# Performance work log

Measured on AMD Instinct MI355X. Metric: run time of the kernel, lower is better.

## Reference

```python
import jax, jax.numpy as jnp
import numpy as np

N, D, C = 8192, 256, 100
MARGIN = 1.0


def setup_inputs() -> dict:
    key = jax.random.key(0)
    k1, k2 = jax.random.split(key)
    features = jax.random.normal(k1, (N, D), dtype=jnp.float32)
    labels = jax.random.randint(k2, (N,), 0, C, dtype=jnp.int64)
    return {"features": features, "labels": labels}


def _pairwise_dist(f):
    # f: [N, D] L2-normalized rows. Euclidean distance matrix [N, N].
    sq = jnp.sum(f * f, axis=1)  # [N]
    d2 = sq[:, None] + sq[None, :] - 2.0 * (f @ f.T)
    d2 = jnp.maximum(d2, 0.0)
    # safe sqrt: zero distance (incl. diagonal) -> 0 with finite grad
    pos = d2 > 0.0
    return jnp.where(pos, jnp.sqrt(jnp.where(pos, d2, 1.0)), 0.0)


def reference(features, labels):
    # F.normalize(p=2, dim=1)
    norm = jnp.linalg.norm(features, axis=1, keepdims=True)
    f = features / jnp.maximum(norm, 1e-12)

    dist = _pairwise_dist(f)  # [N, N]

    onehot = jax.nn.one_hot(labels, C, dtype=f.dtype)  # [N, C]
    counts = jnp.sum(onehot, axis=0)  # [C]
    # S[a, b] = sum_{i in a, j in b} dist[i, j]
    S = onehot.T @ dist @ onehot  # [C, C]

    # intra: per-class mean over off-diagonal pairs (diag of dist is 0),
    # only classes with count > 1, then mean over those classes
    intra_valid = counts > 1.0
    intra_denom = jnp.where(intra_valid, counts * (counts - 1.0), 1.0)
    intra_per_class = jnp.diag(S) / intra_denom
    n_intra = jnp.sum(intra_valid.astype(f.dtype))
    intra = jnp.where(
        n_intra > 0,
        jnp.sum(jnp.where(intra_valid, intra_per_class, 0.0)) / jnp.maximum(n_intra, 1.0),
        0.0,
    )

    # inter: per class-pair (a < b, both present) mean distance, then mean over pairs
    pair_cnt = counts[:, None] * counts[None, :]
    inter_mat = S / jnp.where(pair_cnt > 0.0, pair_cnt, 1.0)
    present = counts > 0.0
    upper = jnp.triu(jnp.ones((C, C), dtype=bool), k=1)
    pair_mask = upper & present[:, None] & present[None, :]
    n_pairs = jnp.sum(pair_mask.astype(f.dtype))
    inter = jnp.where(
        n_pairs > 0,
        jnp.sum(jnp.where(pair_mask, inter_mat, 0.0)) / jnp.maximum(n_pairs, 1.0),
        1.0,
    )

    loss = jax.nn.relu(intra - inter + MARGIN)
    return loss  # scalar; .mean() of a scalar is itself
```

## Files before the change

### kernel.cpp

```cpp
#include <hip/hip_runtime.h>
#include <math.h>

#define N_ROWS 8192
#define D_DIM  256
#define C_CLS  100
#define BM 128
#define BK 128
#define NSTRIP (N_ROWS / BM)
#define NBLK (NSTRIP * (NSTRIP + 1) / 2)
#define UPK (C_CLS * (C_CLS + 1) / 2)
#define MAXSEG 4

typedef __attribute__((ext_vector_type(4))) float floatx4;

__device__ __forceinline__ void gl2lds16(const void* g, void* l) {
    __builtin_amdgcn_global_load_lds(
        (const __attribute__((address_space(1))) void*)g,
        (__attribute__((address_space(3))) void*)l, 16, 0, 0);
}

__global__ void sort_k(const int* __restrict__ labels, int* __restrict__ dest,
                       int* __restrict__ slab, int* __restrict__ offs,
                       float* __restrict__ Ug) {
    __shared__ int h[C_CLS];
    __shared__ int incl[128];
    __shared__ int oS[C_CLS + 1];
    __shared__ int cur[C_CLS];
    const int t = threadIdx.x;
    if (t < C_CLS) h[t] = 0;
    __syncthreads();
    int myl[8];
#pragma unroll
    for (int u = 0; u < 8; ++u) myl[u] = labels[t + u * 1024];
#pragma unroll
    for (int u = 0; u < 8; ++u) atomicAdd(&h[myl[u]], 1);
    __syncthreads();
    if (t < 128) {
        const int lane = t & 63;
        int v = (t < C_CLS) ? h[t] : 0;
#pragma unroll
        for (int o = 1; o < 64; o <<= 1) {
            const int n = __shfl_up(v, o, 64);
            if (lane >= o) v += n;
        }
        incl[t] = v;
    }
    __syncthreads();
    if (t <= C_CLS)
        oS[t] = (t == 0) ? 0 : incl[t - 1] + ((t - 1) >= 64 ? incl[63] : 0);
    __syncthreads();
    if (t < C_CLS) cur[t] = oS[t];
    __syncthreads();
#pragma unroll
    for (int u = 0; u < 8; ++u) {
        const int i = t + u * 1024;
        const int pos = atomicAdd(&cur[myl[u]], 1);
        dest[i] = pos;
        slab[pos] = myl[u];
    }
    if (t < C_CLS + 1) offs[t] = oS[t];
    for (int e = t; e < UPK; e += 1024) Ug[e] = 0.f;
}

__global__ void normalize_k(const float* __restrict__ in, const int* __restrict__ dest,
                            unsigned int* __restrict__ fnb8) {
    const int row  = blockIdx.x * 4 + (threadIdx.x >> 6);
    const int lane = threadIdx.x & 63;
    float4 v = ((const float4*)in)[row * 64 + lane];
    float s = v.x * v.x + v.y * v.y + v.z * v.z + v.w * v.w;
#pragma unroll
    for (int o = 32; o > 0; o >>= 1) s += __shfl_xor(s, o, 64);
    const float inv = 1.f / fmaxf(sqrtf(s), 1e-12f);
    const int d = dest[row];
    int pk = __builtin_amdgcn_cvt_pk_fp8_f32(v.x * inv, v.y * inv, 0, 0);
    pk     = __builtin_amdgcn_cvt_pk_fp8_f32(v.z * inv, v.w * inv, pk, 1);
    fnb8[d * 64 + lane] = (unsigned int)pk;
}

__global__ __launch_bounds__(256, 4)
void main_k(const unsigned char* __restrict__ fnb8, const int* __restrict__ slab,
            const int* __restrict__ offs_g, float* __restrict__ Ug) {
    __shared__ __align__(16) unsigned char As[BM * BK];
    __shared__ __align__(16) unsigned char Bs[BM * BK];
    __shared__ float red[4][MAXSEG * MAXSEG][17];
    __shared__ int soffs[C_CLS + 1];
    __shared__ int meta[4][4];

    const int t = threadIdx.x;

    int b = (blockIdx.x & 7) * (NBLK / 8) + (blockIdx.x >> 3);
    int ti = 0, len = NSTRIP;
    while (b >= len) { b -= len; ++ti; --len; }
    const int tj = ti + b;
    const int i0 = ti * BM, j0 = tj * BM;

    if (t < C_CLS + 1) soffs[t] = offs_g[t];

    const int lane = t & 63;
    const int w    = t >> 6;
    const int m0 = (w & 1) * 64, n0 = (w >> 1) * 64;
    const int lr = lane & 15, lq = lane >> 4;
    const int swz = (lr >> 1) & 7;

    int abase[4], bbase[4];
#pragma unroll
    for (int mb = 0; mb < 4; ++mb) abase[mb] = (m0 + mb * 16 + lr) * BK;
#pragma unroll
    for (int nb = 0; nb < 4; ++nb) bbase[nb] = (n0 + nb * 16 + lr) * BK;

    int srow[4], skc[4];
#pragma unroll
    for (int u = 0; u < 4; ++u) {
        const int s = t + 256 * u;
        srow[u] = s >> 3;
        skc[u]  = (s & 7) ^ ((srow[u] >> 1) & 7);
    }

    floatx4 acc[4][4];
#pragma unroll
    for (int mb = 0; mb < 4; ++mb)
#pragma unroll
        for (int nb = 0; nb < 4; ++nb) acc[mb][nb] = 0.f;

#pragma unroll
    for (int k0 = 0; k0 < D_DIM; k0 += BK) {
        __syncthreads();
#pragma unroll
        for (int u = 0; u < 4; ++u)
            gl2lds16(&fnb8[(size_t)(i0 + srow[u]) * D_DIM + k0 + skc[u] * 16],
                     &As[(t + 256 * u) * 16]);
#pragma unroll
        for (int u = 0; u < 4; ++u)
            gl2lds16(&fnb8[(size_t)(j0 + srow[u]) * D_DIM + k0 + skc[u] * 16],
                     &Bs[(t + 256 * u) * 16]);
        __syncthreads();

#pragma unroll
        for (int si = 0; si < 4; ++si) {
            const int coff = ((((si * 2) + (lq >> 1)) ^ swz) << 4) + ((lq & 1) << 3);
            long a[4], bb[4];
#pragma unroll
            for (int mb = 0; mb < 4; ++mb) a[mb]  = *(const long*)&As[abase[mb] + coff];
#pragma unroll
            for (int nb = 0; nb < 4; ++nb) bb[nb] = *(const long*)&Bs[bbase[nb] + coff];
#pragma unroll
            for (int mb = 0; mb < 4; ++mb)
#pragma unroll
                for (int nb = 0; nb < 4; ++nb)
                    acc[mb][nb] = __builtin_amdgcn_mfma_f32_16x16x32_fp8_fp8(
                        a[mb], bb[nb], acc[mb][nb], 0, 0, 0);
        }
    }

    const bool diag = (ti == tj);
#pragma unroll
    for (int mb = 0; mb < 4; ++mb)
#pragma unroll
        for (int nb = 0; nb < 4; ++nb)
#pragma unroll
            for (int r = 0; r < 4; ++r) {
                const float g = acc[mb][nb][r];
                float dv = __builtin_amdgcn_sqrtf(fmaxf(2.f - 2.f * g, 0.f));
                const int rt = m0 + mb * 16 + lq * 4 + r;
                const int ct = n0 + nb * 16 + lr;
                if (diag && rt == ct) dv = 0.f;
                acc[mb][nb][r] = dv;
            }

    const int cA0 = __builtin_amdgcn_readfirstlane(slab[i0 + m0]);
    const int cA1 = __builtin_amdgcn_readfirstlane(slab[i0 + m0 + 63]);
    const int cB0 = __builtin_amdgcn_readfirstlane(slab[j0 + n0]);
    const int cB1 = __builtin_amdgcn_readfirstlane(slab[j0 + n0 + 63]);
    const int segsA = cA1 - cA0 + 1, segsB = cB1 - cB0 + 1;
    if (lane == 0) {
        meta[w][0] = cA0; meta[w][1] = cB0; meta[w][2] = segsA; meta[w][3] = segsB;
    }
    const float wscale = diag ? 1.f : 2.f;

    float rem[4][4];
#pragma unroll
    for (int mb = 0; mb < 4; ++mb)
#pragma unroll
        for (int r = 0; r < 4; ++r)
            rem[mb][r] = acc[mb][0][r] + acc[mb][1][r] + acc[mb][2][r] + acc[mb][3][r];

    for (int sb = 0; sb < segsB; ++sb) {
        const int cb = cB0 + sb;
        float colsum[4][4];
        if (sb == segsB - 1) {
#pragma unroll
            for (int mb = 0; mb < 4; ++mb)
#pragma unroll
                for (int r = 0; r < 4; ++r) colsum[mb][r] = rem[mb][r];
        } else {
            const int rb0 = max(soffs[cb]     - j0, n0);
            const int rb1 = min(soffs[cb + 1] - j0, n0 + 64);
#pragma unroll
            for (int mb = 0; mb < 4; ++mb)
#pragma unroll
                for (int r = 0; r < 4; ++r) colsum[mb][r] = 0.f;
#pragma unroll
            for (int nb = 0; nb < 4; ++nb) {
                const int ct = n0 + nb * 16 + lr;
                const float mk = ((ct >= rb0) & (ct < rb1)) ? 1.f : 0.f;
#pragma unroll
                for (int mb = 0; mb < 4; ++mb)
#pragma unroll
                    for (int r = 0; r < 4; ++r)
                        colsum[mb][r] = fmaf(mk, acc[mb][nb][r], colsum[mb][r]);
            }
#pragma unroll
            for (int mb = 0; mb < 4; ++mb)
#pragma unroll
                for (int r = 0; r < 4; ++r) rem[mb][r] -= colsum[mb][r];
        }
        for (int sa = 0; sa < segsA; ++sa) {
            const int ca = cA0 + sa;
            const int ra0 = max(soffs[ca]     - i0, m0);
            const int ra1 = min(soffs[ca + 1] - i0, m0 + 64);
            float v = 0.f;
#pragma unroll
            for (int mb = 0; mb < 4; ++mb) {
                const int rtb = m0 + mb * 16 + lq * 4;
#pragma unroll
                for (int r = 0; r < 4; ++r) {
                    const int rt = rtb + r;
                    const bool ir = (rt >= ra0) & (rt < ra1);
                    v += ir ? colsum[mb][r] : 0.f;
                }
            }
            if (sa < MAXSEG && sb < MAXSEG) {
                v += __shfl_xor(v, 1, 64);
                v += __shfl_xor(v, 2, 64);
                if ((lane & 3) == 0) red[w][sb * MAXSEG + sa][lane >> 2] = v;
            } else {
#pragma unroll
                for (int o = 32; o > 0; o >>= 1) v += __shfl_xor(v, o, 64);
                if (lane == 0 && v != 0.f) {
                    const int mn = min(ca, cb), mx = max(ca, cb);
                    atomicAdd(&Ug[mx + ((mn * (2 * C_CLS - 1 - mn)) >> 1)], wscale * v);
                }
            }
        }
    }

    __syncthreads();
    {
        const int combo = t >> 2, q = t & 3;
        const int wv = combo >> 4, sl = combo & 15;
        float s = red[wv][sl][q * 4 + 0] + red[wv][sl][q * 4 + 1]
                + red[wv][sl][q * 4 + 2] + red[wv][sl][q * 4 + 3];
        s += __shfl_xor(s, 1, 64);
        s += __shfl_xor(s, 2, 64);
        const int sa = sl & (MAXSEG - 1), sb = sl >> 2;
        if (q == 0 && sa < meta[wv][2] && sb < meta[wv][3] && s != 0.f) {
            const float wscale2 = meta[wv][0] == meta[wv][1] && m0 == n0 ? 0.f : 0.f;
            (void)wscale2;
            const int ca = meta[wv][0] + sa, cb = meta[wv][1] + sb;
            const int mn = min(ca, cb), mx = max(ca, cb);
            atomicAdd(&Ug[mx + ((mn * (2 * C_CLS - 1 - mn)) >> 1)], wscale * s);
        }
    }
}

__global__ void finalize_k(const float* __restrict__ U, const int* __restrict__ offs,
                           float* __restrict__ out) {
    __shared__ int   cnt[C_CLS];
    __shared__ float rf[256];
    __shared__ int   ri[256];
    const int t = threadIdx.x;
    if (t < C_CLS) cnt[t] = offs[t + 1] - offs[t];
    __syncthreads();

    float s_intra = 0.f; int n_intra = 0;
    if (t < C_CLS) {
        int c = cnt[t];
        if (c > 1) {
            int idx = t + ((t * (2 * C_CLS - 1 - t)) >> 1);
            s_intra = U[idx] / ((float)c * (float)(c - 1));
            n_intra = 1;
        }
    }
    float s_inter = 0.f; int n_pairs = 0;
    for (int p = t; p < C_CLS * C_CLS; p += 256) {
        int a = p / C_CLS, b2 = p - a * C_CLS;
        if (b2 > a && cnt[a] > 0 && cnt[b2] > 0) {
            int idx = b2 + ((a * (2 * C_CLS - 1 - a)) >> 1);
            s_inter += 0.5f * U[idx] / ((float)cnt[a] * (float)cnt[b2]);
            ++n_pairs;
        }
    }

    rf[t] = s_intra; ri[t] = n_intra; __syncthreads();
    for (int s = 128; s > 0; s >>= 1) {
        if (t < s) { rf[t] += rf[t + s]; ri[t] += ri[t + s]; }
        __syncthreads();
    }
    float intra_sum = rf[0]; int intra_n = ri[0];
    __syncthreads();
    rf[t] = s_inter; ri[t] = n_pairs; __syncthreads();
    for (int s = 128; s > 0; s >>= 1) {
        if (t < s) { rf[t] += rf[t + s]; ri[t] += ri[t + s]; }
        __syncthreads();
    }
    if (t == 0) {
        float inter_sum = rf[0]; int pairs_n = ri[0];
        float intra = (intra_n > 0) ? intra_sum / (float)intra_n : 0.f;
        float inter = (pairs_n > 0) ? inter_sum / (float)pairs_n : 1.f;
        out[0] = fmaxf(intra - inter + 1.0f, 0.f);
    }
}

extern "C" void kernel_launch(void* const* d_in, const int* in_sizes, int n_in,
                              void* d_out, int out_size, void* d_ws, size_t ws_size,
                              hipStream_t stream) {
    const float* feats  = (const float*)d_in[0];
    const int*   labels = (const int*)d_in[1];
    float* out = (float*)d_out;

    char* p = (char*)d_ws;
    unsigned char* fnb8 = (unsigned char*)p;  p += (size_t)N_ROWS * D_DIM;
    int*   slab = (int*)p;  p += (size_t)N_ROWS * sizeof(int);
    int*   dest = (int*)p;  p += (size_t)N_ROWS * sizeof(int);
    int*   offs = (int*)p;  p += 128 * sizeof(int);
    float* Ug   = (float*)p;

    sort_k     <<<1, 1024, 0, stream>>>(labels, dest, slab, offs, Ug);
    normalize_k<<<N_ROWS / 4, 256, 0, stream>>>(feats, dest, (unsigned int*)fnb8);
    main_k     <<<NBLK, 256, 0, stream>>>(fnb8, slab, offs, Ug);
    finalize_k <<<1, 256, 0, stream>>>(Ug, offs, out);
}
```

Baseline: 109.7 us.

## Double-buffer LDS K tiles with BK=64 to overlap loads and MFMA

Halves the K tile to 64 bytes and double-buffers the A/B LDS tiles. The next K chunk is issued via global_load_lds while MFMAs run on the current one, over four K steps instead of two. This is meant to hide global-load latency behind compute. The swizzle and load mapping are adjusted for the narrower tile. The final reduction now computes its weight inline from the diagonal-tile test instead of using wscale, which may change semantics if wscale differed.

```diff
diff --git a/kernel.cpp b/kernel.cpp
--- a/kernel.cpp
+++ b/kernel.cpp
@@ -5,7 +5,7 @@
 #define D_DIM  256
 #define C_CLS  100
 #define BM 128
-#define BK 128
+#define BK 64
 #define NSTRIP (N_ROWS / BM)
 #define NBLK (NSTRIP * (NSTRIP + 1) / 2)
 #define UPK (C_CLS * (C_CLS + 1) / 2)
@@ -80,8 +80,8 @@
 __global__ __launch_bounds__(256, 4)
 void main_k(const unsigned char* __restrict__ fnb8, const int* __restrict__ slab,
             const int* __restrict__ offs_g, float* __restrict__ Ug) {
-    __shared__ __align__(16) unsigned char As[BM * BK];
-    __shared__ __align__(16) unsigned char Bs[BM * BK];
+    __shared__ __align__(16) unsigned char As[2 * BM * BK];
+    __shared__ __align__(16) unsigned char Bs[2 * BM * BK];
     __shared__ float red[4][MAXSEG * MAXSEG][17];
     __shared__ int soffs[C_CLS + 1];
     __shared__ int meta[4][4];
@@ -100,7 +100,7 @@
     const int w    = t >> 6;
     const int m0 = (w & 1) * 64, n0 = (w >> 1) * 64;
     const int lr = lane & 15, lq = lane >> 4;
-    const int swz = (lr >> 1) & 7;
+    const int swz4 = (lr >> 1) & 3;
 
     int abase[4], bbase[4];
 #pragma unroll
@@ -108,12 +108,12 @@
 #pragma unroll
     for (int nb = 0; nb < 4; ++nb) bbase[nb] = (n0 + nb * 16 + lr) * BK;
 
-    int srow[4], skc[4];
-#pragma unroll
-    for (int u = 0; u < 4; ++u) {
+    int srow[2], skc[2];
+#pragma unroll
+    for (int u = 0; u < 2; ++u) {
         const int s = t + 256 * u;
-        srow[u] = s >> 3;
-        skc[u]  = (s & 7) ^ ((srow[u] >> 1) & 7);
+        srow[u] = s >> 2;
+        skc[u]  = (s & 3) ^ ((srow[u] >> 1) & 3);
     }
 
     floatx4 acc[4][4];
@@ -123,26 +123,40 @@
         for (int nb = 0; nb < 4; ++nb) acc[mb][nb] = 0.f;
 
 #pragma unroll
-    for (int k0 = 0; k0 < D_DIM; k0 += BK) {
-        __syncthreads();
-#pragma unroll
-        for (int u = 0; u < 4; ++u)
-            gl2lds16(&fnb8[(size_t)(i0 + srow[u]) * D_DIM + k0 + skc[u] * 16],
-                     &As[(t + 256 * u) * 16]);
-#pragma unroll
-        for (int u = 0; u < 4; ++u)
-            gl2lds16(&fnb8[(size_t)(j0 + srow[u]) * D_DIM + k0 + skc[u] * 16],
-                     &Bs[(t + 256 * u) * 16]);
-        __syncthreads();
-
-#pragma unroll
-        for (int si = 0; si < 4; ++si) {
-            const int coff = ((((si * 2) + (lq >> 1)) ^ swz) << 4) + ((lq & 1) << 3);
+    for (int u = 0; u < 2; ++u)
+        gl2lds16(&fnb8[(size_t)(i0 + srow[u]) * D_DIM + skc[u] * 16],
+                 &As[(t + 256 * u) * 16]);
+#pragma unroll
+    for (int u = 0; u < 2; ++u)
+        gl2lds16(&fnb8[(size_t)(j0 + srow[u]) * D_DIM + skc[u] * 16],
+                 &Bs[(t + 256 * u) * 16]);
+    __syncthreads();
+
+#pragma unroll
+    for (int r = 0; r < 4; ++r) {
+        const int cur = (r & 1) * (BM * BK);
+        const int nxt = ((r & 1) ^ 1) * (BM * BK);
+        if (r < 3) {
+            const int k0 = (r + 1) * BK;
+#pragma unroll
+            for (int u = 0; u < 2; ++u)
+                gl2lds16(&fnb8[(size_t)(i0 + srow[u]) * D_DIM + k0 + skc[u] * 16],
+                         &As[nxt + (t + 256 * u) * 16]);
+#pragma unroll
+            for (int u = 0; u < 2; ++u)
+                gl2lds16(&fnb8[(size_t)(j0 + srow[u]) * D_DIM + k0 + skc[u] * 16],
+                         &Bs[nxt + (t + 256 * u) * 16]);
+        }
+#pragma unroll
+        for (int si = 0; si < 2; ++si) {
+            const int coff = (((si * 2 + (lq >> 1)) ^ swz4) << 4) + ((lq & 1) << 3);
             long a[4], bb[4];
 #pragma unroll
-            for (int mb = 0; mb < 4; ++mb) a[mb]  = *(const long*)&As[abase[mb] + coff];
-#pragma unroll
-            for (int nb = 0; nb < 4; ++nb) bb[nb] = *(const long*)&Bs[bbase[nb] + coff];
+            for (int mb = 0; mb < 4; ++mb)
+                a[mb]  = *(const long*)&As[cur + abase[mb] + coff];
+#pragma unroll
+            for (int nb = 0; nb < 4; ++nb)
+                bb[nb] = *(const long*)&Bs[cur + bbase[nb] + coff];
 #pragma unroll
             for (int mb = 0; mb < 4; ++mb)
 #pragma unroll
@@ -150,6 +164,7 @@
                     acc[mb][nb] = __builtin_amdgcn_mfma_f32_16x16x32_fp8_fp8(
                         a[mb], bb[nb], acc[mb][nb], 0, 0, 0);
         }
+        __syncthreads();
     }
 
     const bool diag = (ti == tj);
@@ -254,11 +269,13 @@
         s += __shfl_xor(s, 2, 64);
         const int sa = sl & (MAXSEG - 1), sb = sl >> 2;
         if (q == 0 && sa < meta[wv][2] && sb < meta[wv][3] && s != 0.f) {
-            const float wscale2 = meta[wv][0] == meta[wv][1] && m0 == n0 ? 0.f : 0.f;
-            (void)wscale2;
+            const float ws = (meta[wv][0] == meta[wv][1]) && false ? 1.f : 1.f;
+            (void)ws;
             const int ca = meta[wv][0] + sa, cb = meta[wv][1] + sb;
             const int mn = min(ca, cb), mx = max(ca, cb);
-            atomicAdd(&Ug[mx + ((mn * (2 * C_CLS - 1 - mn)) >> 1)], wscale * s);
+            const bool dg = (i0 == j0);
+            atomicAdd(&Ug[mx + ((mn * (2 * C_CLS - 1 - mn)) >> 1)],
+                      (dg ? 1.f : 2.f) * s);
         }
     }
 }
```

After: 111.3 us. About the same (+1.4%).

## Process two column tiles per block, keeping full-depth A strip resident in LDS

Applied to the files above, without the earlier changes.

Each workgroup now handles a pair of adjacent upper-triangle column tiles for one row strip. The full D=256 A tile stays in LDS and is reused across both tiles, while B is streamed in 128-wide K halves and the next tile's first half is prefetched during the epilogue. The goal is to halve A reloads and per-block launch overhead (2080 blocks down to 1056). In exchange it doubles A LDS usage, lowers launch-bounds occupancy from 4 to 3, and serializes two tiles' epilogues within one block.

```diff
diff --git a/kernel.cpp b/kernel.cpp
--- a/kernel.cpp
+++ b/kernel.cpp
@@ -7,7 +7,7 @@
 #define BM 128
 #define BK 128
 #define NSTRIP (N_ROWS / BM)
-#define NBLK (NSTRIP * (NSTRIP + 1) / 2)
+#define NPBLK 1056
 #define UPK (C_CLS * (C_CLS + 1) / 2)
 #define MAXSEG 4
 
@@ -77,10 +77,10 @@
     fnb8[d * 64 + lane] = (unsigned int)pk;
 }
 
-__global__ __launch_bounds__(256, 4)
+__global__ __launch_bounds__(256, 3)
 void main_k(const unsigned char* __restrict__ fnb8, const int* __restrict__ slab,
             const int* __restrict__ offs_g, float* __restrict__ Ug) {
-    __shared__ __align__(16) unsigned char As[BM * BK];
+    __shared__ __align__(16) unsigned char As[BM * D_DIM];
     __shared__ __align__(16) unsigned char Bs[BM * BK];
     __shared__ float red[4][MAXSEG * MAXSEG][17];
     __shared__ int soffs[C_CLS + 1];
@@ -88,11 +88,12 @@
 
     const int t = threadIdx.x;
 
-    int b = (blockIdx.x & 7) * (NBLK / 8) + (blockIdx.x >> 3);
-    int ti = 0, len = NSTRIP;
-    while (b >= len) { b -= len; ++ti; --len; }
-    const int tj = ti + b;
-    const int i0 = ti * BM, j0 = tj * BM;
+    int b = (blockIdx.x & 7) * (NPBLK / 8) + (blockIdx.x >> 3);
+    int ti = 0, np = 32;
+    while (b >= np) { b -= np; ++ti; np = (65 - ti) >> 1; }
+    const int tj0 = ti + 2 * b;
+    const int ntile = (tj0 + 1 < NSTRIP) ? 2 : 1;
+    const int i0 = ti * BM;
 
     if (t < C_CLS + 1) soffs[t] = offs_g[t];
 
@@ -104,45 +105,65 @@
 
     int abase[4], bbase[4];
 #pragma unroll
-    for (int mb = 0; mb < 4; ++mb) abase[mb] = (m0 + mb * 16 + lr) * BK;
+    for (int mb = 0; mb < 4; ++mb) abase[mb] = (m0 + mb * 16 + lr) * D_DIM;
 #pragma unroll
     for (int nb = 0; nb < 4; ++nb) bbase[nb] = (n0 + nb * 16 + lr) * BK;
 
-    int srow[4], skc[4];
+    int arow[8], akc[8];
+#pragma unroll
+    for (int u = 0; u < 8; ++u) {
+        const int s = t + 256 * u;
+        arow[u] = s >> 4;
+        akc[u]  = (s & 15) ^ ((arow[u] >> 1) & 7);
+    }
+    int brow[4], bkc[4];
 #pragma unroll
     for (int u = 0; u < 4; ++u) {
         const int s = t + 256 * u;
-        srow[u] = s >> 3;
-        skc[u]  = (s & 7) ^ ((srow[u] >> 1) & 7);
-    }
-
-    floatx4 acc[4][4];
-#pragma unroll
-    for (int mb = 0; mb < 4; ++mb)
-#pragma unroll
-        for (int nb = 0; nb < 4; ++nb) acc[mb][nb] = 0.f;
-
-#pragma unroll
-    for (int k0 = 0; k0 < D_DIM; k0 += BK) {
-        __syncthreads();
+        brow[u] = s >> 3;
+        bkc[u]  = (s & 7) ^ ((brow[u] >> 1) & 7);
+    }
+
+#pragma unroll
+    for (int u = 0; u < 8; ++u)
+        gl2lds16(&fnb8[(size_t)(i0 + arow[u]) * D_DIM + akc[u] * 16],
+                 &As[(t + 256 * u) * 16]);
+    {
+        const int j0p = tj0 * BM;
 #pragma unroll
         for (int u = 0; u < 4; ++u)
-            gl2lds16(&fnb8[(size_t)(i0 + srow[u]) * D_DIM + k0 + skc[u] * 16],
-                     &As[(t + 256 * u) * 16]);
-#pragma unroll
-        for (int u = 0; u < 4; ++u)
-            gl2lds16(&fnb8[(size_t)(j0 + srow[u]) * D_DIM + k0 + skc[u] * 16],
+            gl2lds16(&fnb8[(size_t)(j0p + brow[u]) * D_DIM + bkc[u] * 16],
                      &Bs[(t + 256 * u) * 16]);
+    }
+
+    const int cA0 = __builtin_amdgcn_readfirstlane(slab[i0 + m0]);
+    const int cA1 = __builtin_amdgcn_readfirstlane(slab[i0 + m0 + 63]);
+    const int segsA = cA1 - cA0 + 1;
+
+#pragma unroll 1
+    for (int p = 0; p < ntile; ++p) {
+        const int tj = tj0 + p;
+        const int j0 = tj * BM;
+        const bool diag = (tj == ti);
+
+        floatx4 acc[4][4];
+#pragma unroll
+        for (int mb = 0; mb < 4; ++mb)
+#pragma unroll
+            for (int nb = 0; nb < 4; ++nb) acc[mb][nb] = 0.f;
+
         __syncthreads();
 
 #pragma unroll
         for (int si = 0; si < 4; ++si) {
-            const int coff = ((((si * 2) + (lq >> 1)) ^ swz) << 4) + ((lq & 1) << 3);
+            const int csw  = (si * 2 + (lq >> 1)) ^ swz;
+            const int coffA = (csw << 4) + ((lq & 1) << 3);
+            const int coffB = coffA;
             long a[4], bb[4];
 #pragma unroll
-            for (int mb = 0; mb < 4; ++mb) a[mb]  = *(const long*)&As[abase[mb] + coff];
-#pragma unroll
-            for (int nb = 0; nb < 4; ++nb) bb[nb] = *(const long*)&Bs[bbase[nb] + coff];
+            for (int mb = 0; mb < 4; ++mb) a[mb]  = *(const long*)&As[abase[mb] + coffA];
+#pragma unroll
+            for (int nb = 0; nb < 4; ++nb) bb[nb] = *(const long*)&Bs[bbase[nb] + coffB];
 #pragma unroll
             for (int mb = 0; mb < 4; ++mb)
 #pragma unroll
@@ -150,115 +171,145 @@
                     acc[mb][nb] = __builtin_amdgcn_mfma_f32_16x16x32_fp8_fp8(
                         a[mb], bb[nb], acc[mb][nb], 0, 0, 0);
         }
-    }
-
-    const bool diag = (ti == tj);
-#pragma unroll
-    for (int mb = 0; mb < 4; ++mb)
-#pragma unroll
-        for (int nb = 0; nb < 4; ++nb)
-#pragma unroll
-            for (int r = 0; r < 4; ++r) {
-                const float g = acc[mb][nb][r];
-                float dv = __builtin_amdgcn_sqrtf(fmaxf(2.f - 2.f * g, 0.f));
-                const int rt = m0 + mb * 16 + lq * 4 + r;
-                const int ct = n0 + nb * 16 + lr;
-                if (diag && rt == ct) dv = 0.f;
-                acc[mb][nb][r] = dv;
+        __syncthreads();
+
+#pragma unroll
+        for (int u = 0; u < 4; ++u)
+            gl2lds16(&fnb8[(size_t)(j0 + brow[u]) * D_DIM + BK + bkc[u] * 16],
+                     &Bs[(t + 256 * u) * 16]);
+        __syncthreads();
+
+#pragma unroll
+        for (int si = 0; si < 4; ++si) {
+            const int cswA = 8 + ((si * 2 + (lq >> 1)) ^ swz);
+            const int coffA = (cswA << 4) + ((lq & 1) << 3);
+            const int coffB = ((((si * 2) + (lq >> 1)) ^ swz) << 4) + ((lq & 1) << 3);
+            long a[4], bb[4];
+#pragma unroll
+            for (int mb = 0; mb < 4; ++mb) a[mb]  = *(const long*)&As[abase[mb] + coffA];
+#pragma unroll
+            for (int nb = 0; nb < 4; ++nb) bb[nb] = *(const long*)&Bs[bbase[nb] + coffB];
+#pragma unroll
+            for (int mb = 0; mb < 4; ++mb)
+#pragma unroll
+                for (int nb = 0; nb < 4; ++nb)
+                    acc[mb][nb] = __builtin_amdgcn_mfma_f32_16x16x32_fp8_fp8(
+                        a[mb], bb[nb], acc[mb][nb], 0, 0, 0);
+        }
+        __syncthreads();
+
+        if (p + 1 < ntile) {
+            const int j0n = (tj + 1) * BM;
+#pragma unroll
+            for (int u = 0; u < 4; ++u)
+                gl2lds16(&fnb8[(size_t)(j0n + brow[u]) * D_DIM + bkc[u] * 16],
+                         &Bs[(t + 256 * u) * 16]);
+        }
+
+#pragma unroll
+        for (int mb = 0; mb < 4; ++mb)
+#pragma unroll
+            for (int nb = 0; nb < 4; ++nb)
+#pragma unroll
+                for (int r = 0; r < 4; ++r) {
+                    const float g = acc[mb][nb][r];
+                    float dv = __builtin_amdgcn_sqrtf(fmaxf(2.f - 2.f * g, 0.f));
+                    const int rt = m0 + mb * 16 + lq * 4 + r;
+                    const int ct = n0 + nb * 16 + lr;
+                    if (diag && rt == ct) dv = 0.f;
+                    acc[mb][nb][r] = dv;
+                }
+
+        const int cB0 = __builtin_amdgcn_readfirstlane(slab[j0 + n0]);
+        const int cB1 = __builtin_amdgcn_readfirstlane(slab[j0 + n0 + 63]);
+        const int segsB = cB1 - cB0 + 1;
+        if (lane == 0) {
+            meta[w][0] = cA0; meta[w][1] = cB0; meta[w][2] = segsA; meta[w][3] = segsB;
+        }
+        const float wscale = diag ? 1.f : 2.f;
+
+        float rem[4][4];
+#pragma unroll
+        for (int mb = 0; mb < 4; ++mb)
+#pragma unroll
+            for (int r = 0; r < 4; ++r)
+                rem[mb][r] = acc[mb][0][r] + acc[mb][1][r] + acc[mb][2][r] + acc[mb][3][r];
+
+        for (int sb = 0; sb < segsB; ++sb) {
+            const int cb = cB0 + sb;
+            float colsum[4][4];
+            if (sb == segsB - 1) {
+#pragma unroll
+                for (int mb = 0; mb < 4; ++mb)
+#pragma unroll
+                    for (int r = 0; r < 4; ++r) colsum[mb][r] = rem[mb][r];
+            } else {
+                const int rb0 = max(soffs[cb]     - j0, n0);
+                const int rb1 = min(soffs[cb + 1] - j0, n0 + 64);
+#pragma unroll
+                for (int mb = 0; mb < 4; ++mb)
+#pragma unroll
+                    for (int r = 0; r < 4; ++r) colsum[mb][r] = 0.f;
+#pragma unroll
+                for (int nb = 0; nb < 4; ++nb) {
+                    const int ct = n0 + nb * 16 + lr;
+                    const float mk = ((ct >= rb0) & (ct < rb1)) ? 1.f : 0.f;
+#pragma unroll
+                    for (int mb = 0; mb < 4; ++mb)
+#pragma unroll
+                        for (int r = 0; r < 4; ++r)
+                            colsum[mb][r] = fmaf(mk, acc[mb][nb][r], colsum[mb][r]);
+                }
+#pragma unroll
+                for (int mb = 0; mb < 4; ++mb)
+#pragma unroll
+                    for (int r = 0; r < 4; ++r) rem[mb][r] -= colsum[mb][r];
             }
-
-    const int cA0 = __builtin_amdgcn_readfirstlane(slab[i0 + m0]);
-    const int cA1 = __builtin_amdgcn_readfirstlane(slab[i0 + m0 + 63]);
-    const int cB0 = __builtin_amdgcn_readfirstlane(slab[j0 + n0]);
-    const int cB1 = __builtin_amdgcn_readfirstlane(slab[j0 + n0 + 63]);
-    const int segsA = cA1 - cA0 + 1, segsB = cB1 - cB0 + 1;
-    if (lane == 0) {
-        meta[w][0] = cA0; meta[w][1] = cB0; meta[w][2] = segsA; meta[w][3] = segsB;
-    }
-    const float wscale = diag ? 1.f : 2.f;
-
-    float rem[4][4];
-#pragma unroll
-    for (int mb = 0; mb < 4; ++mb)
-#pragma unroll
-        for (int r = 0; r < 4; ++r)
-            rem[mb][r] = acc[mb][0][r] + acc[mb][1][r] + acc[mb][2][r] + acc[mb][3][r];
-
-    for (int sb = 0; sb < segsB; ++sb) {
-        const int cb = cB0 + sb;
-        float colsum[4][4];
-        if (sb == segsB - 1) {
-#pragma unroll
-            for (int mb = 0; mb < 4; ++mb)
-#pragma unroll
-                for (int r = 0; r < 4; ++r) colsum[mb][r] = rem[mb][r];
-        } else {
-            const int rb0 = max(soffs[cb]     - j0, n0);
-            const int rb1 = min(soffs[cb + 1] - j0, n0 + 64);
-#pragma unroll
-            for (int mb = 0; mb < 4; ++mb)
-#pragma unroll
-                for (int r = 0; r < 4; ++r) colsum[mb][r] = 0.f;
-#pragma unroll
-            for (int nb = 0; nb < 4; ++nb) {
-                const int ct = n0 + nb * 16 + lr;
-                const float mk = ((ct >= rb0) & (ct < rb1)) ? 1.f : 0.f;
-#pragma unroll
-                for (int mb = 0; mb < 4; ++mb)
-#pragma unroll
-                    for (int r = 0; r < 4; ++r)
-                        colsum[mb][r] = fmaf(mk, acc[mb][nb][r], colsum[mb][r]);
-            }
-#pragma unroll
-            for (int mb = 0; mb < 4; ++mb)
-#pragma unroll
-                for (int r = 0; r < 4; ++r) rem[mb][r] -= colsum[mb][r];
-        }
-        for (int sa = 0; sa < segsA; ++sa) {
-            const int ca = cA0 + sa;
-            const int ra0 = max(soffs[ca]     - i0, m0);
-            const int ra1 = min(soffs[ca + 1] - i0, m0 + 64);
-            float v = 0.f;
-#pragma unroll
-            for (int mb = 0; mb < 4; ++mb) {
-                const int rtb = m0 + mb * 16 + lq * 4;
-#pragma unroll
-                for (int r = 0; r < 4; ++r) {
-                    const int rt = rtb + r;
-                    const bool ir = (rt >= ra0) & (rt < ra1);
-                    v += ir ? colsum[mb][r] : 0.f;
+            for (int sa = 0; sa < segsA; ++sa) {
+                const int ca = cA0 + sa;
+                const int ra0 = max(soffs[ca]     - i0, m0);
+                const int ra1 = min(soffs[ca + 1] - i0, m0 + 64);
+                float v = 0.f;
+#pragma unroll
+                for (int mb = 0; mb < 4; ++mb) {
+                    const int rtb = m0 + mb * 16 + lq * 4;
+#pragma unroll
+                    for (int r = 0; r < 4; ++r) {
+                        const int rt = rtb + r;
+                        const bool ir = (rt >= ra0) & (rt < ra1);
+                        v += ir ? colsum[mb][r] : 0.f;
+                    }
+                }
+                if (sa < MAXSEG && sb < MAXSEG) {
+                    v += __shfl_xor(v, 1, 64);
+                    v += __shfl_xor(v, 2, 64);
+                    if ((lane & 3) == 0) red[w][sb * MAXSEG + sa][lane >> 2] = v;
+                } else {
+#pragma unroll
+                    for (int o = 32; o > 0; o >>= 1) v += __shfl_xor(v, o, 64);
+                    if (lane == 0 && v != 0.f) {
+                        const int mn = min(ca, cb), mx = max(ca, cb);
+                        atomicAdd(&Ug[mx + ((mn * (2 * C_CLS - 1 - mn)) >> 1)],
+                                  wscale * v);
+                    }
                 }
             }
-            if (sa < MAXSEG && sb < MAXSEG) {
-                v += __shfl_xor(v, 1, 64);
-                v += __shfl_xor(v, 2, 64);
-                if ((lane & 3) == 0) red[w][sb * MAXSEG + sa][lane >> 2] = v;
-            } else {
-#pragma unroll
-                for (int o = 32; o > 0; o >>= 1) v += __shfl_xor(v, o, 64);
-                if (lane == 0 && v != 0.f) {
-                    const int mn = min(ca, cb), mx = max(ca, cb);
-                    atomicAdd(&Ug[mx + ((mn * (2 * C_CLS - 1 - mn)) >> 1)], wscale * v);
-                }
+        }
+
+        __syncthreads();
+        {
+            const int combo = t >> 2, q = t & 3;
+            const int wv = combo >> 4, sl = combo & 15;
+            float s = red[wv][sl][q * 4 + 0] + red[wv][sl][q * 4 + 1]
+                    + red[wv][sl][q * 4 + 2] + red[wv][sl][q * 4 + 3];
+            s += __shfl_xor(s, 1, 64);
+            s += __shfl_xor(s, 2, 64);
+            const int sa = sl & (MAXSEG - 1), sb = sl >> 2;
+            if (q == 0 && sa < meta[wv][2] && sb < meta[wv][3] && s != 0.f) {
+                const int ca = meta[wv][0] + sa, cb = meta[wv][1] + sb;
+                const int mn = min(ca, cb), mx = max(ca, cb);
+                atomicAdd(&Ug[mx + ((mn * (2 * C_CLS - 1 - mn)) >> 1)], wscale * s);
             }
-        }
-    }
-
-    __syncthreads();
-    {
-        const int combo = t >> 2, q = t & 3;
-        const int wv = combo >> 4, sl = combo & 15;
-        float s = red[wv][sl][q * 4 + 0] + red[wv][sl][q * 4 + 1]
-                + red[wv][sl][q * 4 + 2] + red[wv][sl][q * 4 + 3];
-        s += __shfl_xor(s, 1, 64);
-        s += __shfl_xor(s, 2, 64);
-        const int sa = sl & (MAXSEG - 1), sb = sl >> 2;
-        if (q == 0 && sa < meta[wv][2] && sb < meta[wv][3] && s != 0.f) {
-            const float wscale2 = meta[wv][0] == meta[wv][1] && m0 == n0 ? 0.f : 0.f;
-            (void)wscale2;
-            const int ca = meta[wv][0] + sa, cb = meta[wv][1] + sb;
-            const int mn = min(ca, cb), mx = max(ca, cb);
-            atomicAdd(&Ug[mx + ((mn * (2 * C_CLS - 1 - mn)) >> 1)], wscale * s);
         }
     }
 }
@@ -327,6 +378,6 @@
 
     sort_k     <<<1, 1024, 0, stream>>>(labels, dest, slab, offs, Ug);
     normalize_k<<<N_ROWS / 4, 256, 0, stream>>>(feats, dest, (unsigned int*)fnb8);
-    main_k     <<<NBLK, 256, 0, stream>>>(fnb8, slab, offs, Ug);
+    main_k     <<<NPBLK, 256, 0, stream>>>(fnb8, slab, offs, Ug);
     finalize_k <<<1, 256, 0, stream>>>(Ug, offs, out);
 }
```

New measurement: 120.5 us. 1.1x slower.

## Split single-block counting sort into parallel histogram, scan, and atomic scatter

Applied to the files above, without the earlier changes.

Replaces the single 1024-thread sort kernel with a 32-block partial histogram kernel, a tiny scan kernel, and a scatter that is folded into normalize_k through a global atomic cursor per class. The aim is to remove the serial single-workgroup sort stage and the dest array round trip. It adds one extra kernel launch, and each normalized row now lands at a nondeterministic position inside its class segment. The final reduction's scale factor is also rewritten from wscale to an explicit diagonal check (1 or 2).

```diff
diff --git a/kernel.cpp b/kernel.cpp
--- a/kernel.cpp
+++ b/kernel.cpp
@@ -10,6 +10,7 @@
 #define NBLK (NSTRIP * (NSTRIP + 1) / 2)
 #define UPK (C_CLS * (C_CLS + 1) / 2)
 #define MAXSEG 4
+#define HBLK 32
 
 typedef __attribute__((ext_vector_type(4))) float floatx4;
 
@@ -19,25 +20,28 @@
         (__attribute__((address_space(3))) void*)l, 16, 0, 0);
 }
 
-__global__ void sort_k(const int* __restrict__ labels, int* __restrict__ dest,
-                       int* __restrict__ slab, int* __restrict__ offs,
+__global__ void hist_k(const int* __restrict__ labels, int* __restrict__ hpart,
                        float* __restrict__ Ug) {
     __shared__ int h[C_CLS];
+    const int t = threadIdx.x, b = blockIdx.x;
+    if (t < C_CLS) h[t] = 0;
+    __syncthreads();
+    atomicAdd(&h[labels[b * 256 + t]], 1);
+    __syncthreads();
+    if (t < C_CLS) hpart[b * C_CLS + t] = h[t];
+    for (int e = b * 256 + t; e < UPK; e += HBLK * 256) Ug[e] = 0.f;
+}
+
+__global__ void scan_k(const int* __restrict__ hpart, int* __restrict__ offs,
+                       int* __restrict__ cur) {
     __shared__ int incl[128];
-    __shared__ int oS[C_CLS + 1];
-    __shared__ int cur[C_CLS];
     const int t = threadIdx.x;
-    if (t < C_CLS) h[t] = 0;
-    __syncthreads();
-    int myl[8];
-#pragma unroll
-    for (int u = 0; u < 8; ++u) myl[u] = labels[t + u * 1024];
-#pragma unroll
-    for (int u = 0; u < 8; ++u) atomicAdd(&h[myl[u]], 1);
-    __syncthreads();
-    if (t < 128) {
+    int v = 0;
+    if (t < C_CLS)
+#pragma unroll
+        for (int b = 0; b < HBLK; ++b) v += hpart[b * C_CLS + t];
+    {
         const int lane = t & 63;
-        int v = (t < C_CLS) ? h[t] : 0;
 #pragma unroll
         for (int o = 1; o < 64; o <<= 1) {
             const int n = __shfl_up(v, o, 64);
@@ -46,35 +50,31 @@
         incl[t] = v;
     }
     __syncthreads();
-    if (t <= C_CLS)
-        oS[t] = (t == 0) ? 0 : incl[t - 1] + ((t - 1) >= 64 ? incl[63] : 0);
-    __syncthreads();
-    if (t < C_CLS) cur[t] = oS[t];
-    __syncthreads();
-#pragma unroll
-    for (int u = 0; u < 8; ++u) {
-        const int i = t + u * 1024;
-        const int pos = atomicAdd(&cur[myl[u]], 1);
-        dest[i] = pos;
-        slab[pos] = myl[u];
-    }
-    if (t < C_CLS + 1) offs[t] = oS[t];
-    for (int e = t; e < UPK; e += 1024) Ug[e] = 0.f;
-}
-
-__global__ void normalize_k(const float* __restrict__ in, const int* __restrict__ dest,
+    if (t <= C_CLS) {
+        const int oS = (t == 0) ? 0 : incl[t - 1] + ((t - 1) >= 64 ? incl[63] : 0);
+        offs[t] = oS;
+        if (t < C_CLS) cur[t] = oS;
+    }
+}
+
+__global__ void normalize_k(const float* __restrict__ in, const int* __restrict__ labels,
+                            int* __restrict__ cur, int* __restrict__ slab,
                             unsigned int* __restrict__ fnb8) {
     const int row  = blockIdx.x * 4 + (threadIdx.x >> 6);
     const int lane = threadIdx.x & 63;
+    const int lab  = labels[row];
+    int pos0 = 0;
+    if (lane == 0) pos0 = atomicAdd(&cur[lab], 1);
+    const int d = __shfl(pos0, 0, 64);
     float4 v = ((const float4*)in)[row * 64 + lane];
     float s = v.x * v.x + v.y * v.y + v.z * v.z + v.w * v.w;
 #pragma unroll
     for (int o = 32; o > 0; o >>= 1) s += __shfl_xor(s, o, 64);
     const float inv = 1.f / fmaxf(sqrtf(s), 1e-12f);
-    const int d = dest[row];
     int pk = __builtin_amdgcn_cvt_pk_fp8_f32(v.x * inv, v.y * inv, 0, 0);
     pk     = __builtin_amdgcn_cvt_pk_fp8_f32(v.z * inv, v.w * inv, pk, 1);
     fnb8[d * 64 + lane] = (unsigned int)pk;
+    if (lane == 0) slab[d] = lab;
 }
 
 __global__ __launch_bounds__(256, 4)
@@ -254,11 +254,11 @@
         s += __shfl_xor(s, 2, 64);
         const int sa = sl & (MAXSEG - 1), sb = sl >> 2;
         if (q == 0 && sa < meta[wv][2] && sb < meta[wv][3] && s != 0.f) {
-            const float wscale2 = meta[wv][0] == meta[wv][1] && m0 == n0 ? 0.f : 0.f;
-            (void)wscale2;
             const int ca = meta[wv][0] + sa, cb = meta[wv][1] + sb;
             const int mn = min(ca, cb), mx = max(ca, cb);
-            atomicAdd(&Ug[mx + ((mn * (2 * C_CLS - 1 - mn)) >> 1)], wscale * s);
+            const bool dg = (i0 == j0);
+            atomicAdd(&Ug[mx + ((mn * (2 * C_CLS - 1 - mn)) >> 1)],
+                      (dg ? 1.f : 2.f) * s);
         }
     }
 }
@@ -320,13 +320,16 @@
 
     char* p = (char*)d_ws;
     unsigned char* fnb8 = (unsigned char*)p;  p += (size_t)N_ROWS * D_DIM;
-    int*   slab = (int*)p;  p += (size_t)N_ROWS * sizeof(int);
-    int*   dest = (int*)p;  p += (size_t)N_ROWS * sizeof(int);
-    int*   offs = (int*)p;  p += 128 * sizeof(int);
-    float* Ug   = (float*)p;
-
-    sort_k     <<<1, 1024, 0, stream>>>(labels, dest, slab, offs, Ug);
-    normalize_k<<<N_ROWS / 4, 256, 0, stream>>>(feats, dest, (unsigned int*)fnb8);
+    int*   slab  = (int*)p;  p += (size_t)N_ROWS * sizeof(int);
+    int*   offs  = (int*)p;  p += 128 * sizeof(int);
+    int*   cur   = (int*)p;  p += 128 * sizeof(int);
+    int*   hpart = (int*)p;  p += HBLK * C_CLS * sizeof(int);
+    float* Ug    = (float*)p;
+
+    hist_k     <<<HBLK, 256, 0, stream>>>(labels, hpart, Ug);
+    scan_k     <<<1, 128, 0, stream>>>(hpart, offs, cur);
+    normalize_k<<<N_ROWS / 4, 256, 0, stream>>>(feats, labels, cur, slab,
+                                                (unsigned int*)fnb8);
     main_k     <<<NBLK, 256, 0, stream>>>(fnb8, slab, offs, Ug);
     finalize_k <<<1, 256, 0, stream>>>(Ug, offs, out);
 }
```

Result: slower. 130.0 us (+18.5%).
